# Performance work log

Hardware: AMD Instinct MI355X
Metric: run time of the kernel (lower is better)

## Reference

```python
import jax, jax.numpy as jnp
import numpy as np

DIM = 2048
HEAD_DIM = 64
NUM_HEADS = DIM // HEAD_DIM
ROT_DIM = HEAD_DIM // 2  # 32
THETA = 10000.0
LN_EPS = 1e-5


def setup_inputs() -> dict:
    key = jax.random.key(0)
    ks = jax.random.split(key, 6)
    n, s = 2, 2048
    x = jax.random.normal(ks[0], (n, s, DIM), dtype=jnp.float32)
    ln_w = jnp.ones((DIM,), dtype=jnp.float32)
    ln_b = jnp.zeros((DIM,), dtype=jnp.float32)
    # Linear weights stored as (in, out); torch Linear init scale ~ 1/sqrt(in)
    sc = 1.0 / np.sqrt(DIM)
    w_qkv = jax.random.uniform(ks[1], (DIM, 3 * DIM), jnp.float32, -sc, sc)
    b_qkv = jax.random.uniform(ks[2], (3 * DIM,), jnp.float32, -sc, sc)
    w_out = jax.random.uniform(ks[3], (DIM, DIM), jnp.float32, -sc, sc)
    b_out = jax.random.uniform(ks[4], (DIM,), jnp.float32, -sc, sc)
    return {"x": x, "ln_w": ln_w, "ln_b": ln_b, "w_qkv": w_qkv,
            "b_qkv": b_qkv, "w_out": w_out, "b_out": b_out}


def _rope_cos_sin(seq_len):
    # freqs: theta ** linspace(0, -1, rot_dim//2 + 1)[:-1] -> 16 freqs
    n_freq = ROT_DIM // 2
    exps = jnp.linspace(0.0, -1.0, n_freq + 1)[:-1]
    freqs = THETA ** exps  # [16]
    pos = jnp.arange(seq_len, dtype=jnp.float32)  # [s]
    tmp = pos[:, None] * freqs[None, :]  # [s, 16]
    # broadcast target: [1, 1, s, 16] over (n, h, s, d)
    return jnp.cos(tmp)[None, None], jnp.sin(tmp)[None, None]


def _apply_rotary(x, cos, sin):
    d = cos.shape[-1]  # 16
    x1, x2, x3 = x[..., :d], x[..., d:2 * d], x[..., 2 * d:]
    y1 = x1 * cos - x2 * sin
    y2 = x2 * cos + x1 * sin
    return jnp.concatenate([y1.astype(x3.dtype), y2.astype(x3.dtype), x3], axis=-1)


def reference(x, ln_w, ln_b, w_qkv, b_qkv, w_out, b_out):
    n, s, dim = x.shape
    skip = x
    # LayerNorm
    mu = jnp.mean(x, axis=-1, keepdims=True)
    var = jnp.var(x, axis=-1, keepdims=True)
    h = (x - mu) * jax.lax.rsqrt(var + LN_EPS) * ln_w + ln_b
    # fused QKV projection
    qkv = h @ w_qkv + b_qkv  # [n, s, 3*dim]
    qkv = qkv.reshape(n, s, 3, NUM_HEADS, HEAD_DIM)
    qkv = jnp.transpose(qkv, (2, 0, 3, 1, 4))  # [3, n, h, s, d]
    q, k, v = qkv[0], qkv[1], qkv[2]
    # RoPE on first rot_dim dims
    cos, sin = _rope_cos_sin(s)
    q = _apply_rotary(q, cos, sin)
    k = _apply_rotary(k, cos, sin)
    # causal SDPA
    scale = 1.0 / jnp.sqrt(jnp.asarray(HEAD_DIM, dtype=q.dtype))
    scores = jnp.einsum('nhqd,nhkd->nhqk', q, k) * scale
    causal = jnp.tril(jnp.ones((s, s), dtype=bool))
    scores = jnp.where(causal[None, None], scores, jnp.asarray(-jnp.inf, scores.dtype))
    attn = jax.nn.softmax(scores, axis=-1)
    o = jnp.einsum('nhqk,nhkd->nhqd', attn, v)  # [n, h, s, d]
    o = jnp.transpose(o, (0, 2, 1, 3)).reshape(n, s, dim)
    return o @ w_out + b_out + skip
```

## Files before the change

### kernel.cpp

```cpp
#include <hip/hip_runtime.h>
#include <hip/hip_bf16.h>
#include <cstdint>
#include <cstddef>

#define DIMM 2048
#define NHEADS 32
#define HDIM 64
#define SEQ 2048
#define NBATCH 2
#define ROWS 4096
#define NFREQ 16
#define NKT3 32

typedef __bf16 bfv8 __attribute__((ext_vector_type(8)));
typedef float f32x4v __attribute__((ext_vector_type(4)));
typedef float f32x16 __attribute__((ext_vector_type(16)));

__device__ __forceinline__ void gload16(const void* g, void* l) {
  __builtin_amdgcn_global_load_lds((const __attribute__((address_space(1))) void*)g,
                                   (__attribute__((address_space(3))) void*)l, 16, 0, 0);
}

__device__ __forceinline__ f32x4v mfma16(bfv8 a, bfv8 b, f32x4v c) {
  return __builtin_amdgcn_mfma_f32_16x16x32_bf16(a, b, c, 0, 0, 0);
}

__device__ __forceinline__ f32x16 mfma32(bfv8 a, bfv8 b, f32x16 c) {
  return __builtin_amdgcn_mfma_f32_32x32x16_bf16(a, b, c, 0, 0, 0);
}

__device__ __forceinline__ unsigned short f2bfu(float f) {
  __hip_bfloat16 h = __float2bfloat16(f);
  return __builtin_bit_cast(unsigned short, h);
}

__device__ __forceinline__ unsigned pack2bf(float a, float b) {
  return (unsigned)f2bfu(a) | ((unsigned)f2bfu(b) << 16);
}

__device__ __forceinline__ void swap32(unsigned& a, unsigned& b, const int hi) {
  const unsigned ta = (unsigned)__shfl_xor((int)a, 32);
  const unsigned tb = (unsigned)__shfl_xor((int)b, 32);
  const unsigned na = hi ? tb : a;
  const unsigned nb = hi ? b : ta;
  a = na;
  b = nb;
}

__device__ __forceinline__ void xcd_swizzle(int& bx, int& by) {
  const int gx = gridDim.x, nwg = gx * gridDim.y;
  const int orig = blockIdx.y * gx + blockIdx.x;
  const int q = nwg >> 3, r = nwg & 7;
  const int xcd = orig & 7, loc = orig >> 3;
  const int wg = (xcd < r ? xcd * (q + 1) : r * (q + 1) + (xcd - r) * q) + loc;
  bx = wg % gx;
  by = wg / gx;
}

__global__ __launch_bounds__(256) void rope_tab_kernel(float* __restrict__ ct,
                                                       float* __restrict__ st) {
  const int i = blockIdx.x * 256 + threadIdx.x;
  if (i >= SEQ * NFREQ) return;
  const int pos = i >> 4, f = i & 15;
  const float freq = powf(10000.0f, -(float)f / 16.0f);
  const float ang = (float)pos * freq;
  ct[i] = cosf(ang);
  st[i] = sinf(ang);
}

__global__ __launch_bounds__(256) void transpose_cast_kernel(const float* __restrict__ W,
                                                             __hip_bfloat16* __restrict__ WT,
                                                             int K, int N) {
  __shared__ float tile[32][33];
  const int n0 = blockIdx.x * 32, k0 = blockIdx.y * 32;
  const int tx = threadIdx.x, ty = threadIdx.y;
#pragma unroll
  for (int j = 0; j < 4; ++j)
    tile[ty + j * 8][tx] = W[(size_t)(k0 + ty + j * 8) * N + n0 + tx];
  __syncthreads();
#pragma unroll
  for (int j = 0; j < 4; ++j)
    WT[(size_t)(n0 + ty + j * 8) * K + k0 + tx] = __float2bfloat16(tile[tx][ty + j * 8]);
}

__global__ __launch_bounds__(256) void ln_kernel(const float* __restrict__ x,
                                                 const float* __restrict__ lw,
                                                 const float* __restrict__ lb,
                                                 __hip_bfloat16* __restrict__ h) {
  const int row = blockIdx.x;
  const int t = threadIdx.x;
  const float4* xr = (const float4*)(x + (size_t)row * DIMM);
  float4 a = xr[t * 2], b = xr[t * 2 + 1];
  float e[8];
  *(float4*)e = a; *(float4*)(e + 4) = b;
  float s = 0.f, ss = 0.f;
#pragma unroll
  for (int j = 0; j < 8; ++j) { s += e[j]; ss += e[j] * e[j]; }
#pragma unroll
  for (int o = 1; o < 64; o <<= 1) { s += __shfl_xor(s, o); ss += __shfl_xor(ss, o); }
  __shared__ float red[8];
  const int wid = t >> 6;
  if ((t & 63) == 0) { red[wid * 2] = s; red[wid * 2 + 1] = ss; }
  __syncthreads();
  s = red[0] + red[2] + red[4] + red[6];
  ss = red[1] + red[3] + red[5] + red[7];
  const float mu = s * (1.f / DIMM);
  const float var = ss * (1.f / DIMM) - mu * mu;
  const float rs = rsqrtf(var + 1e-5f);
  const float4* w4 = (const float4*)lw;
  const float4* b4 = (const float4*)lb;
  float4 wa = w4[t * 2], wb = w4[t * 2 + 1], ba = b4[t * 2], bb = b4[t * 2 + 1];
  float wv[8], bv[8];
  *(float4*)wv = wa; *(float4*)(wv + 4) = wb;
  *(float4*)bv = ba; *(float4*)(bv + 4) = bb;
  unsigned short hv[8];
#pragma unroll
  for (int j = 0; j < 8; ++j)
    hv[j] = f2bfu((e[j] - mu) * rs * wv[j] + bv[j]);
  *(uint4*)((char*)h + (size_t)row * (DIMM * 2) + t * 16) = *(uint4*)hv;
}

__device__ __forceinline__ void stageA64(const char* Ab, int brow, int kt,
                                         char* bufA, int c, int lane) {
  const int row = c * 8 + (lane >> 3);
  const int src = ((lane & 7) * 16) ^ ((row & 7) << 4);
  gload16(Ab + (size_t)(brow + row) * 4096 + kt * 128 + src, bufA + c * 1024);
}
__device__ __forceinline__ void stageB64(const char* Bb, int bcol, int kt,
                                         char* bufB, int c, int lane) {
  const int row = c * 8 + (lane >> 3);
  const int src = ((lane & 7) * 16) ^ ((row & 7) << 4);
  gload16(Bb + (size_t)(bcol + row) * 4096 + kt * 128 + src, bufB + c * 1024);
}

__device__ __forceinline__ void gemm_core3(const char* Ab, const char* Bb,
                                           int brow, int bcol, char* lds,
                                           f32x4v acc[8][4]) {
  const int tid = threadIdx.x, lane = tid & 63, wid = tid >> 6;
  const int g = lane >> 4, ln15 = lane & 15;
  const int wr = wid >> 2, wc = (wid >> 1) & 1, wk = wid & 1;
  const int kb = wk * 64;

#pragma unroll
  for (int t = 0; t < 2; ++t) {
    char* bufA = lds + t * 49152;
    char* bufB = bufA + 32768;
    stageA64(Ab, brow, t, bufA, wid, lane);
    stageA64(Ab, brow, t, bufA, wid + 8, lane);
    stageA64(Ab, brow, t, bufA, wid + 16, lane);
    stageA64(Ab, brow, t, bufA, wid + 24, lane);
    stageB64(Bb, bcol, t, bufB, wid, lane);
    stageB64(Bb, bcol, t, bufB, wid + 8, lane);
  }
  asm volatile("s_waitcnt vmcnt(6)" ::: "memory");
  __builtin_amdgcn_s_barrier();

  for (int t = 0; t < NKT3; ++t) {
    char* bufA = lds + (t % 3) * 49152;
    char* bufB = bufA + 32768;
    char* nbufA = lds + ((t + 2) % 3) * 49152;
    char* nbufB = nbufA + 32768;
    const bool st = (t + 2 < NKT3);
    bfv8 af[4], bfr[4];
#pragma unroll
    for (int mi = 0; mi < 4; ++mi) {
      const int ra = wr * 128 + mi * 16 + ln15;
      af[mi] = *(const bfv8*)(bufA + (size_t)ra * 128 + ((kb + g * 16) ^ ((ra & 7) << 4)));
    }
#pragma unroll
    for (int nf = 0; nf < 4; ++nf) {
      const int rb = wc * 64 + nf * 16 + ln15;
      bfr[nf] = *(const bfv8*)(bufB + (size_t)rb * 128 + ((kb + g * 16) ^ ((rb & 7) << 4)));
    }
    if (st) {
      stageA64(Ab, brow, t + 2, nbufA, wid, lane);
      stageA64(Ab, brow, t + 2, nbufA, wid + 8, lane);
      stageB64(Bb, bcol, t + 2, nbufB, wid, lane);
    }
    asm volatile("s_waitcnt lgkmcnt(0)" ::: "memory");
    __builtin_amdgcn_sched_barrier(0);
    __builtin_amdgcn_s_setprio(1);
#pragma unroll
    for (int mi = 0; mi < 4; ++mi)
#pragma unroll
      for (int nf = 0; nf < 4; ++nf)
        acc[mi][nf] = mfma16(af[mi], bfr[nf], acc[mi][nf]);
    __builtin_amdgcn_s_setprio(0);
    bfv8 ao[4];
#pragma unroll
    for (int mi = 0; mi < 4; ++mi) {
      const int ra = wr * 128 + (4 + mi) * 16 + ln15;
      ao[mi] = *(const bfv8*)(bufA + (size_t)ra * 128 + ((kb + g * 16) ^ ((ra & 7) << 4)));
    }
    if (st) {
      stageA64(Ab, brow, t + 2, nbufA, wid + 16, lane);
      stageA64(Ab, brow, t + 2, nbufA, wid + 24, lane);
      stageB64(Bb, bcol, t + 2, nbufB, wid + 8, lane);
    }
    asm volatile("s_waitcnt lgkmcnt(0)" ::: "memory");
    __builtin_amdgcn_sched_barrier(0);
    __builtin_amdgcn_s_setprio(1);
#pragma unroll
    for (int mi = 0; mi < 4; ++mi)
#pragma unroll
      for (int nf = 0; nf < 4; ++nf)
        acc[4 + mi][nf] = mfma16(ao[mi], bfr[nf], acc[4 + mi][nf]);
    __builtin_amdgcn_s_setprio(0);
    if (st) {
      asm volatile("s_waitcnt vmcnt(6)" ::: "memory");
    } else if (t == NKT3 - 2) {
      asm volatile("s_waitcnt vmcnt(0)" ::: "memory");
    }
    __builtin_amdgcn_s_barrier();
  }
}

__device__ __forceinline__ void kreduce(char* lds, f32x4v acc[8][4], f32x4v ak[4][4],
                                        int wid, int lane, int wk) {
  char* reg = lds + (size_t)wid * 16384;
#pragma unroll
  for (int q = 0; q < 4; ++q)
#pragma unroll
    for (int nf = 0; nf < 4; ++nf)
      *(f32x4v*)(reg + (q * 4 + nf) * 1024 + lane * 16) = acc[wk ? q : 4 + q][nf];
  __syncthreads();
  const char* preg = lds + (size_t)(wid ^ 1) * 16384;
#pragma unroll
  for (int q = 0; q < 4; ++q)
#pragma unroll
    for (int nf = 0; nf < 4; ++nf)
      ak[q][nf] = acc[wk ? 4 + q : q][nf] +
                  *(const f32x4v*)(preg + (q * 4 + nf) * 1024 + lane * 16);
  __syncthreads();
}

__global__ __launch_bounds__(512, 2) void gemm_qkv_kernel(
    const __hip_bfloat16* __restrict__ A, const __hip_bfloat16* __restrict__ BT,
    const float* __restrict__ bqkv, const float* __restrict__ ct, const float* __restrict__ st,
    __hip_bfloat16* __restrict__ qb, __hip_bfloat16* __restrict__ kb,
    __hip_bfloat16* __restrict__ vb) {
  __shared__ char lds[147456];
  const f32x4v fz = {0.f, 0.f, 0.f, 0.f};
  f32x4v acc[8][4];
#pragma unroll
  for (int mf = 0; mf < 8; ++mf)
#pragma unroll
    for (int nf = 0; nf < 4; ++nf) acc[mf][nf] = fz;
  int bx, by;
  xcd_swizzle(bx, by);
  const int brow = by * 256, bcol = bx * 128;
  gemm_core3((const char*)A, (const char*)BT, brow, bcol, lds, acc);

  const int tid = threadIdx.x, lane = tid & 63, wid = tid >> 6;
  const int g = lane >> 4, ln15 = lane & 15;
  const int wr = wid >> 2, wc = (wid >> 1) & 1, wk = wid & 1;
  f32x4v ak[4][4];
  kreduce(lds, acc, ak, wid, lane, wk);

  const int cb = bcol + wc * 64;
  const int which = cb >> 11;
  const int head = (cb & 2047) >> 6;
  const int rowbase = brow + wr * 128 + wk * 64;
  float bias[4];
#pragma unroll
  for (int nf = 0; nf < 4; ++nf) bias[nf] = bqkv[cb + nf * 16 + ln15];

  if (which == 2) {
    char* tp = lds + wid * 8192;
    const int nidx = brow >> 11;
    const size_t vhead = ((size_t)nidx * NHEADS + head) * (HDIM * SEQ);
    const int posb = (rowbase & 2047);
#pragma unroll
    for (int q = 0; q < 4; ++q)
#pragma unroll
      for (int r = 0; r < 4; ++r) {
        const int posl = q * 16 + g * 4 + r;
#pragma unroll
        for (int nf = 0; nf < 4; ++nf) {
          const int d = nf * 16 + ln15;
          *(unsigned short*)(tp + d * 128 + ((posl * 2) ^ ((d & 7) << 4))) =
              f2bfu(ak[q][nf][r] + bias[nf]);
        }
      }
    asm volatile("s_waitcnt lgkmcnt(0)" ::: "memory");
    __builtin_amdgcn_sched_barrier(0);
#pragma unroll
    for (int i = 0; i < 8; ++i) {
      const int dl = i * 8 + (lane >> 3);
      const int cs = (lane & 7) ^ (dl & 7);
      const uint4 val = *(const uint4*)(tp + dl * 128 + cs * 16);
      *(uint4*)((char*)vb + (vhead + (size_t)dl * SEQ + posb + (lane & 7) * 8) * 2) = val;
    }
  } else {
    __hip_bfloat16* dst = (which == 0) ? qb : kb;
#pragma unroll
    for (int q = 0; q < 4; ++q)
#pragma unroll
      for (int r = 0; r < 4; ++r) {
        const int row = rowbase + q * 16 + g * 4 + r;
        const int nidx = row >> 11, pos = row & 2047;
        float v0 = ak[q][0][r] + bias[0];
        float v1 = ak[q][1][r] + bias[1];
        float v2 = ak[q][2][r] + bias[2];
        float v3 = ak[q][3][r] + bias[3];
        const float c0 = ct[pos * 16 + ln15], s0 = st[pos * 16 + ln15];
        const float x1 = v0, x2 = v1;
        v0 = x1 * c0 - x2 * s0;
        v1 = x2 * c0 + x1 * s0;
        __hip_bfloat16* p = dst + (((size_t)(nidx * NHEADS + head)) * SEQ + pos) * HDIM;
        p[ln15] = __float2bfloat16(v0);
        p[16 + ln15] = __float2bfloat16(v1);
        p[32 + ln15] = __float2bfloat16(v2);
        p[48 + ln15] = __float2bfloat16(v3);
      }
  }
}

__global__ __launch_bounds__(512, 2) void gemm_out_kernel(
    const __hip_bfloat16* __restrict__ A, const __hip_bfloat16* __restrict__ BT,
    const float* __restrict__ bout, const float* __restrict__ skip,
    float* __restrict__ out) {
  __shared__ char lds[147456];
  const f32x4v fz = {0.f, 0.f, 0.f, 0.f};
  f32x4v acc[8][4];
#pragma unroll
  for (int mf = 0; mf < 8; ++mf)
#pragma unroll
    for (int nf = 0; nf < 4; ++nf) acc[mf][nf] = fz;
  int bx, by;
  xcd_swizzle(bx, by);
  const int brow = by * 256, bcol = bx * 128;
  gemm_core3((const char*)A, (const char*)BT, brow, bcol, lds, acc);

  const int tid = threadIdx.x, lane = tid & 63, wid = tid >> 6;
  const int g = lane >> 4, ln15 = lane & 15;
  const int wr = wid >> 2, wc = (wid >> 1) & 1, wk = wid & 1;
  f32x4v ak[4][4];
  kreduce(lds, acc, ak, wid, lane, wk);

  const int rowbase = brow + wr * 128 + wk * 64;
#pragma unroll
  for (int q = 0; q < 4; ++q)
#pragma unroll
    for (int r = 0; r < 4; ++r) {
      const int row = rowbase + q * 16 + g * 4 + r;
      const float* xr = skip + (size_t)row * DIMM;
      float* orow = out + (size_t)row * DIMM;
#pragma unroll
      for (int nf = 0; nf < 4; ++nf) {
        const int c = bcol + wc * 64 + nf * 16 + ln15;
        orow[c] = ak[q][nf][r] + bout[c] + xr[c];
      }
    }
}

__global__ __launch_bounds__(256) void attn_kernel(
    const __hip_bfloat16* __restrict__ qb, const __hip_bfloat16* __restrict__ kb,
    const __hip_bfloat16* __restrict__ vtb, __hip_bfloat16* __restrict__ ob) {
  __shared__ char sm[33280];
  float* lred = (float*)(sm + 32768);
  const int tid = threadIdx.x, lane = tid & 63, wid = tid >> 6;
  const int ln31 = lane & 31, hi = lane >> 5;
  const int head = blockIdx.x;
  const int qbi = (int)gridDim.y - 1 - (int)blockIdx.y;
  const size_t hb = (size_t)head * (SEQ * HDIM);
  const int q0 = qbi * 128;
  const int qw = q0 + wid * 32;
  const int qg = qw + ln31;
  const int nt = qbi * 2 + 2;
  const char* Kg = (const char*)(kb + hb);
  const char* Vg = (const char*)(vtb + hb);

  bfv8 qf[4];
  {
    const char* Qp = (const char*)(qb + hb) + (size_t)(qw + ln31) * 128 + hi * 16;
#pragma unroll
    for (int j = 0; j < 4; ++j) qf[j] = *(const bfv8*)(Qp + j * 32);
  }

  f32x16 o0, o1;
#pragma unroll
  for (int i = 0; i < 16; ++i) { o0[i] = 0.f; o1[i] = 0.f; }
  float m_run = -1e30f, l_run = 0.f;
  const float scale = 0.125f;
  const int swz = (ln31 & 7) << 4;

#pragma unroll
  for (int i = 0; i < 2; ++i) {
    const int f = (tid + i * 256) * 16;
    const int row = f >> 7;
    const int src = (f & 127) ^ ((row & 7) << 4);
    gload16(Kg + (size_t)row * 128 + src, sm + f);
    gload16(Vg + (size_t)row * 4096 + src, sm + 16384 + f);
  }
  asm volatile("s_waitcnt vmcnt(0)" ::: "memory");
  __syncthreads();

  for (int t = 0; t < nt; ++t) {
    const int kvb = t * 64;
    if (t + 1 < nt) {
      const int nb = (t + 1) & 1;
      const int kvb2 = kvb + 64;
#pragma unroll
      for (int i = 0; i < 2; ++i) {
        const int f = (tid + i * 256) * 16;
        const int row = f >> 7;
        const int src = (f & 127) ^ ((row & 7) << 4);
        gload16(Kg + (size_t)(kvb2 + row) * 128 + src, sm + nb * 8192 + f);
        gload16(Vg + (size_t)row * 4096 + (size_t)kvb2 * 2 + src, sm + 16384 + nb * 8192 + f);
      }
    }
    if (kvb <= qw + 31) {
      const char* ldsK = sm + (t & 1) * 8192;
      const char* ldsV = sm + 16384 + (t & 1) * 8192;
      f32x16 s0, s1;
#pragma unroll
      for (int i = 0; i < 16; ++i) { s0[i] = 0.f; s1[i] = 0.f; }
      __builtin_amdgcn_s_setprio(1);
#pragma unroll
      for (int j = 0; j < 4; ++j) {
        const int byt = j * 32 + hi * 16;
        const bfv8 k0 = *(const bfv8*)(ldsK + ln31 * 128 + (byt ^ swz));
        const bfv8 k1 = *(const bfv8*)(ldsK + (32 + ln31) * 128 + (byt ^ swz));
        s0 = mfma32(k0, qf[j], s0);
        s1 = mfma32(k1, qf[j], s1);
      }
      __builtin_amdgcn_s_setprio(0);
      float p[32];
#pragma unroll
      for (int r = 0; r < 16; ++r) { p[r] = s0[r] * scale; p[16 + r] = s1[r] * scale; }
      if (kvb + 63 > qw) {
#pragma unroll
        for (int r = 0; r < 16; ++r) {
          const int kvo = (r & 3) + 8 * (r >> 2) + 4 * hi;
          if (kvb + kvo > qg) p[r] = -1e30f;
          if (kvb + 32 + kvo > qg) p[16 + r] = -1e30f;
        }
      }
      float mx = p[0];
#pragma unroll
      for (int r = 1; r < 32; ++r) mx = fmaxf(mx, p[r]);
      mx = fmaxf(mx, __shfl_xor(mx, 32));
      if (!__all(mx <= m_run + 8.0f)) {
        const float mn = fmaxf(m_run, mx);
        const float al = __expf(m_run - mn);
        m_run = mn;
        l_run *= al;
        lred[wid * 32 + ln31] = al;
        asm volatile("s_waitcnt lgkmcnt(0)" ::: "memory");
        __builtin_amdgcn_sched_barrier(0);
#pragma unroll
        for (int r = 0; r < 16; ++r) {
          const float a = lred[wid * 32 + (r & 3) + 8 * (r >> 2) + 4 * hi];
          o0[r] *= a;
          o1[r] *= a;
        }
      }
      float ps = 0.f;
#pragma unroll
      for (int r = 0; r < 32; ++r) { p[r] = __expf(p[r] - m_run); ps += p[r]; }
      ps += __shfl_xor(ps, 32);
      l_run += ps;
      unsigned c[16];
#pragma unroll
      for (int i = 0; i < 16; ++i) c[i] = pack2bf(p[2 * i], p[2 * i + 1]);
      bfv8 paf[4];
#pragma unroll
      for (int fI = 0; fI < 4; ++fI) {
        unsigned a0 = c[fI * 4 + 0], b0 = c[fI * 4 + 2];
        unsigned a1 = c[fI * 4 + 1], b1 = c[fI * 4 + 3];
        swap32(a0, b0, hi);
        swap32(a1, b1, hi);
        union { unsigned u[4]; bfv8 v; } w;
        w.u[0] = a0; w.u[1] = a1; w.u[2] = b0; w.u[3] = b1;
        paf[fI] = w.v;
      }
      __builtin_amdgcn_s_setprio(1);
#pragma unroll
      for (int ss = 0; ss < 4; ++ss) {
        const int byt = ss * 32 + hi * 16;
        const bfv8 v0 = *(const bfv8*)(ldsV + ln31 * 128 + (byt ^ swz));
        const bfv8 v1 = *(const bfv8*)(ldsV + (32 + ln31) * 128 + (byt ^ swz));
        o0 = mfma32(paf[ss], v0, o0);
        o1 = mfma32(paf[ss], v1, o1);
      }
      __builtin_amdgcn_s_setprio(0);
    }
    asm volatile("s_waitcnt vmcnt(0)" ::: "memory");
    __syncthreads();
  }

  lred[wid * 32 + ln31] = l_run;
  asm volatile("s_waitcnt lgkmcnt(0)" ::: "memory");
  __builtin_amdgcn_sched_barrier(0);
  const int nidx = head >> 5, hh = head & 31;
#pragma unroll
  for (int r = 0; r < 16; ++r) {
    const int qrow = qw + (r & 3) + 8 * (r >> 2) + 4 * hi;
    const float inv = 1.0f / lred[wid * 32 + (r & 3) + 8 * (r >> 2) + 4 * hi];
    __hip_bfloat16* dst = ob + ((size_t)nidx * SEQ + qrow) * DIMM + hh * 64;
    dst[ln31] = __float2bfloat16(o0[r] * inv);
    dst[32 + ln31] = __float2bfloat16(o1[r] * inv);
  }
}

extern "C" void kernel_launch(void* const* d_in, const int* in_sizes, int n_in,
                              void* d_out, int out_size, void* d_ws, size_t ws_size,
                              hipStream_t stream) {
  const float* x = (const float*)d_in[0];
  const float* ln_w = (const float*)d_in[1];
  const float* ln_b = (const float*)d_in[2];
  const float* w_qkv = (const float*)d_in[3];
  const float* b_qkv = (const float*)d_in[4];
  const float* w_out = (const float*)d_in[5];
  const float* b_out = (const float*)d_in[6];
  float* out = (float*)d_out;

  char* ws = (char*)d_ws;
  size_t off = 0;
  auto alloc = [&](size_t bytes) -> char* {
    char* p = ws + off;
    off += (bytes + 255) & ~(size_t)255;
    return p;
  };
  __hip_bfloat16* h = (__hip_bfloat16*)alloc((size_t)ROWS * DIMM * 2);
  __hip_bfloat16* wqkvT = (__hip_bfloat16*)alloc((size_t)3 * DIMM * DIMM * 2);
  __hip_bfloat16* woutT = (__hip_bfloat16*)alloc((size_t)DIMM * DIMM * 2);
  __hip_bfloat16* qbuf = (__hip_bfloat16*)alloc((size_t)ROWS * DIMM * 2);
  __hip_bfloat16* kbuf = (__hip_bfloat16*)alloc((size_t)ROWS * DIMM * 2);
  __hip_bfloat16* vtbuf = (__hip_bfloat16*)alloc((size_t)ROWS * DIMM * 2);
  __hip_bfloat16* obuf = (__hip_bfloat16*)alloc((size_t)ROWS * DIMM * 2);
  float* ct = (float*)alloc((size_t)SEQ * NFREQ * 4);
  float* st = (float*)alloc((size_t)SEQ * NFREQ * 4);

  rope_tab_kernel<<<dim3((SEQ * NFREQ + 255) / 256), dim3(256), 0, stream>>>(ct, st);
  transpose_cast_kernel<<<dim3(3 * DIMM / 32, DIMM / 32), dim3(32, 8), 0, stream>>>(
      w_qkv, wqkvT, DIMM, 3 * DIMM);
  transpose_cast_kernel<<<dim3(DIMM / 32, DIMM / 32), dim3(32, 8), 0, stream>>>(
      w_out, woutT, DIMM, DIMM);
  ln_kernel<<<dim3(ROWS), dim3(256), 0, stream>>>(x, ln_w, ln_b, h);
  gemm_qkv_kernel<<<dim3(3 * DIMM / 128, ROWS / 256), dim3(512), 0, stream>>>(
      h, wqkvT, b_qkv, ct, st, qbuf, kbuf, vtbuf);
  attn_kernel<<<dim3(NBATCH * NHEADS, SEQ / 128), dim3(256), 0, stream>>>(
      qbuf, kbuf, vtbuf, obuf);
  gemm_out_kernel<<<dim3(DIMM / 128, ROWS / 256), dim3(512), 0, stream>>>(
      obuf, woutT, b_out, x, out);
}
```

Measured before the change: 271.8 us.

## Stage GEMM epilogues through LDS for vectorized stores; drop inner-loop LDS waits

```diff
diff --git a/kernel.cpp b/kernel.cpp
--- a/kernel.cpp
+++ b/kernel.cpp
@@ -177,8 +177,6 @@
       stageA64(Ab, brow, t + 2, nbufA, wid + 8, lane);
       stageB64(Bb, bcol, t + 2, nbufB, wid, lane);
     }
-    asm volatile("s_waitcnt lgkmcnt(0)" ::: "memory");
-    __builtin_amdgcn_sched_barrier(0);
     __builtin_amdgcn_s_setprio(1);
 #pragma unroll
     for (int mi = 0; mi < 4; ++mi)
@@ -197,8 +195,6 @@
       stageA64(Ab, brow, t + 2, nbufA, wid + 24, lane);
       stageB64(Bb, bcol, t + 2, nbufB, wid + 8, lane);
     }
-    asm volatile("s_waitcnt lgkmcnt(0)" ::: "memory");
-    __builtin_amdgcn_sched_barrier(0);
     __builtin_amdgcn_s_setprio(1);
 #pragma unroll
     for (int mi = 0; mi < 4; ++mi)
@@ -211,6 +207,7 @@
     } else if (t == NKT3 - 2) {
       asm volatile("s_waitcnt vmcnt(0)" ::: "memory");
     }
+    asm volatile("" ::: "memory");
     __builtin_amdgcn_s_barrier();
   }
 }
@@ -261,15 +258,15 @@
   const int which = cb >> 11;
   const int head = (cb & 2047) >> 6;
   const int rowbase = brow + wr * 128 + wk * 64;
+  const int nidx = rowbase >> 11;
+  const int posb = rowbase & 2047;
   float bias[4];
 #pragma unroll
   for (int nf = 0; nf < 4; ++nf) bias[nf] = bqkv[cb + nf * 16 + ln15];
 
   if (which == 2) {
     char* tp = lds + wid * 8192;
-    const int nidx = brow >> 11;
     const size_t vhead = ((size_t)nidx * NHEADS + head) * (HDIM * SEQ);
-    const int posb = (rowbase & 2047);
 #pragma unroll
     for (int q = 0; q < 4; ++q)
 #pragma unroll
@@ -293,12 +290,13 @@
     }
   } else {
     __hip_bfloat16* dst = (which == 0) ? qb : kb;
+    char* tp = lds + wid * 8192;
 #pragma unroll
     for (int q = 0; q < 4; ++q)
 #pragma unroll
       for (int r = 0; r < 4; ++r) {
-        const int row = rowbase + q * 16 + g * 4 + r;
-        const int nidx = row >> 11, pos = row & 2047;
+        const int posl = q * 16 + g * 4 + r;
+        const int pos = posb + posl;
         float v0 = ak[q][0][r] + bias[0];
         float v1 = ak[q][1][r] + bias[1];
         float v2 = ak[q][2][r] + bias[2];
@@ -307,12 +305,23 @@
         const float x1 = v0, x2 = v1;
         v0 = x1 * c0 - x2 * s0;
         v1 = x2 * c0 + x1 * s0;
-        __hip_bfloat16* p = dst + (((size_t)(nidx * NHEADS + head)) * SEQ + pos) * HDIM;
-        p[ln15] = __float2bfloat16(v0);
-        p[16 + ln15] = __float2bfloat16(v1);
-        p[32 + ln15] = __float2bfloat16(v2);
-        p[48 + ln15] = __float2bfloat16(v3);
-      }
+        const int sw2 = (posl & 7) << 4;
+        char* rowp = tp + posl * 128;
+        *(unsigned short*)(rowp + ((ln15 * 2) ^ sw2)) = f2bfu(v0);
+        *(unsigned short*)(rowp + ((32 + ln15 * 2) ^ sw2)) = f2bfu(v1);
+        *(unsigned short*)(rowp + ((64 + ln15 * 2) ^ sw2)) = f2bfu(v2);
+        *(unsigned short*)(rowp + ((96 + ln15 * 2) ^ sw2)) = f2bfu(v3);
+      }
+    asm volatile("s_waitcnt lgkmcnt(0)" ::: "memory");
+    __builtin_amdgcn_sched_barrier(0);
+    const size_t qkbase = (((size_t)(nidx * NHEADS + head)) * SEQ + posb) * HDIM;
+#pragma unroll
+    for (int i = 0; i < 8; ++i) {
+      const int rr = i * 8 + (lane >> 3);
+      const int cs = (lane & 7) ^ (rr & 7);
+      const uint4 val = *(const uint4*)(tp + rr * 128 + cs * 16);
+      *(uint4*)((char*)dst + (qkbase + (size_t)rr * HDIM) * 2 + (lane & 7) * 16) = val;
+    }
   }
 }
 
@@ -339,19 +348,38 @@
   kreduce(lds, acc, ak, wid, lane, wk);
 
   const int rowbase = brow + wr * 128 + wk * 64;
+  char* tp = lds + wid * 16384;
 #pragma unroll
   for (int q = 0; q < 4; ++q)
 #pragma unroll
     for (int r = 0; r < 4; ++r) {
-      const int row = rowbase + q * 16 + g * 4 + r;
-      const float* xr = skip + (size_t)row * DIMM;
-      float* orow = out + (size_t)row * DIMM;
-#pragma unroll
-      for (int nf = 0; nf < 4; ++nf) {
-        const int c = bcol + wc * 64 + nf * 16 + ln15;
-        orow[c] = ak[q][nf][r] + bout[c] + xr[c];
-      }
-    }
+      const int posl = q * 16 + g * 4 + r;
+      const int sw2 = ((posl >> 2) & 3) << 6;
+      char* rowp = tp + posl * 256;
+#pragma unroll
+      for (int nf = 0; nf < 4; ++nf)
+        *(float*)(rowp + ((nf * 64 + ln15 * 4) ^ sw2)) = ak[q][nf][r];
+    }
+  asm volatile("s_waitcnt lgkmcnt(0)" ::: "memory");
+  __builtin_amdgcn_sched_barrier(0);
+  const int colb = bcol + wc * 64;
+#pragma unroll
+  for (int i = 0; i < 16; ++i) {
+    const int rr = i * 4 + (lane >> 4);
+    const int cp = lane & 15;
+    const float4 a4 = *(const float4*)(tp + rr * 256 + cp * 16);
+    const int lc = (cp * 16) ^ (((rr >> 2) & 3) << 6);
+    const int col = colb + (lc >> 2);
+    const int row = rowbase + rr;
+    const float4 sk = *(const float4*)(skip + (size_t)row * DIMM + col);
+    const float4 bo = *(const float4*)(bout + col);
+    float4 o4;
+    o4.x = a4.x + sk.x + bo.x;
+    o4.y = a4.y + sk.y + bo.y;
+    o4.z = a4.z + sk.z + bo.z;
+    o4.w = a4.w + sk.w + bo.w;
+    *(float4*)(out + (size_t)row * DIMM + col) = o4;
+  }
 }
 
 __global__ __launch_bounds__(256) void attn_kernel(
```

Measured after the change: 272.1 us. No clear change (+0.1%).
